# Performance work log

Hardware: AMD Instinct MI355X
Metric: run time of the kernel (lower is better)

Reference implementation:

```python
import jax, jax.numpy as jnp
import numpy as np

HEAD = 8

def setup_inputs() -> dict:
    key = jax.random.key(0)
    ks = jax.random.split(key, 11)
    B, C, W, H = 16, 512, 32, 32
    d, N = C // HEAD, W * H
    return {
        "x": jax.random.normal(ks[0], (B, C, W, H), jnp.float32),
        "Wq": jax.random.normal(ks[1], (C, C), jnp.float32) * 0.02,
        "bq": jax.random.normal(ks[2], (C,), jnp.float32) * 0.02,
        "Wk": jax.random.normal(ks[3], (C, C), jnp.float32) * 0.02,
        "bk": jax.random.normal(ks[4], (C,), jnp.float32) * 0.02,
        "Wv": jax.random.normal(ks[5], (C, C), jnp.float32) * 0.02,
        "bv": jax.random.normal(ks[6], (C,), jnp.float32) * 0.02,
        "rel_h": jax.random.normal(ks[7], (1, HEAD, d, 1, H), jnp.float32),
        "rel_w": jax.random.normal(ks[8], (1, HEAD, d, W, 1), jnp.float32),
        "reg_qk": jax.random.normal(ks[9], (1, N, N), jnp.float32),
        "reg_v": jax.random.normal(ks[10], (1, d, N), jnp.float32),
    }

def reference(x, Wq, bq, Wk, bk, Wv, bv, rel_h, rel_w, reg_qk, reg_v):
    B, C, W, H = x.shape
    head = HEAD
    d = C // head
    N = W * H
    def conv1x1(inp, Wt, b):  # 1x1 conv == per-pixel linear
        return jnp.einsum('bchw,oc->bohw', inp, Wt) + b[None, :, None, None]
    q = conv1x1(x, Wq, bq).reshape(B, head, d, N)
    k = conv1x1(x, Wk, bk).reshape(B, head, d, N)
    v = conv1x1(x, Wv, bv).reshape(B, head, d, N)
    # content-content: q^T k -> [B, head, N, N]
    cc = jnp.einsum('bhdn,bhdm->bhnm', q, k)
    # content-position: (rel_h + rel_w) broadcast to [1, head, d, W, H] -> [head, N, d]
    pos = (rel_h + rel_w).reshape(head, d, N)
    cp = jnp.einsum('hdn,bhdm->bhnm', pos, q)
    energy = cc + cp  # [B, head, N, N]
    n_reg = reg_qk.shape[0]
    energy = jnp.concatenate(
        [energy, jnp.broadcast_to(reg_qk[None], (B, n_reg, N, N))], axis=1)
    v_all = jnp.concatenate(
        [v, jnp.broadcast_to(reg_v[None], (B, n_reg, d, N))], axis=1)
    attn = jax.nn.softmax(energy, axis=-1)  # [B, head+n_reg, N, N]
    # v @ attn^T
    out = jnp.einsum('bgdn,bgmn->bgdm', v_all, attn)
    out = out[:, :head].reshape(B, C, W, H)
    return out + x
```

## Files before the change

kernel.cpp:

```cpp
#include <hip/hip_runtime.h>

#define BB   16
#define HEADS 8
#define DH   64
#define NSP  1024
#define CCH  512

typedef unsigned int   u32;
typedef unsigned short u16;
typedef __attribute__((ext_vector_type(8))) short  short8;
typedef __attribute__((ext_vector_type(4))) float  floatx4;

#if defined(__has_builtin)
#if __has_builtin(__builtin_amdgcn_exp2f)
#define EXP2F(x) __builtin_amdgcn_exp2f(x)
#else
#define EXP2F(x) exp2f(x)
#endif
#else
#define EXP2F(x) exp2f(x)
#endif

__device__ __forceinline__ u16 f2b(float f) {
  u32 x = __float_as_uint(f);
  x = x + 0x7fffu + ((x >> 16) & 1u);
  return (u16)(x >> 16);
}

__device__ __forceinline__ u32 pkbf(float lo, float hi) {
  return __builtin_amdgcn_perm(__float_as_uint(hi) + 0x8000u,
                               __float_as_uint(lo) + 0x8000u, 0x07060302u);
}

__device__ __forceinline__ void gload_lds16(const u16* g, u16* l) {
  __builtin_amdgcn_global_load_lds((const __attribute__((address_space(1))) u32*)g,
                                   (__attribute__((address_space(3))) u32*)l, 16, 0, 0);
}

__global__ __launch_bounds__(256) void prep_all(const float* __restrict__ x,
                                                const float* __restrict__ Wq,
                                                const float* __restrict__ Wk,
                                                const float* __restrict__ Wv,
                                                const float* __restrict__ rel_h,
                                                const float* __restrict__ rel_w,
                                                u16* __restrict__ wbf,
                                                u16* __restrict__ pos,
                                                u16* __restrict__ xt) {
  __shared__ float ld[64][68];
  int bid = blockIdx.x;
  int t = threadIdx.x;
  if (bid < 768) {
    int idx = bid * 256 + t;
    int which = idx >> 16;
    int r4 = (idx & 65535) * 4;
    const float* src = which == 0 ? Wq : which == 1 ? Wk : Wv;
    float4 v = *(const float4*)&src[r4];
    ushort4 s;
    s.x = f2b(v.x); s.y = f2b(v.y); s.z = f2b(v.z); s.w = f2b(v.w);
    *(ushort4*)&wbf[(which << 18) + r4] = s;
  } else if (bid < 2816) {
    int idx = (bid - 768) * 256 + t;
    int dd = idx & 63;
    int n  = (idx >> 6) & 1023;
    int h  = idx >> 16;
    int ww = n >> 5, hh = n & 31;
    float v = rel_h[(h * 64 + dd) * 32 + hh] + rel_w[(h * 64 + dd) * 32 + ww];
    pos[idx] = f2b(v);
  } else {
    int bid2 = bid - 2816;
    int ntile = bid2 & 15, ctile = (bid2 >> 4) & 7, b = bid2 >> 7;
    const float* xb = x + (((size_t)b * CCH + ctile * 64) << 10) + ntile * 64;
#pragma unroll
    for (int p = 0; p < 4; ++p) {
      int c = p * 16 + (t >> 4), n4 = (t & 15) * 4;
      float4 v = *(const float4*)&xb[((size_t)c << 10) + n4];
      ld[c][n4 + 0] = v.x; ld[c][n4 + 1] = v.y; ld[c][n4 + 2] = v.z; ld[c][n4 + 3] = v.w;
    }
    __syncthreads();
    u16* xo = xt + (((size_t)b << 10) + ntile * 64) * CCH + ctile * 64;
#pragma unroll
    for (int p = 0; p < 2; ++p) {
      int id = p * 256 + t;
      int n = id >> 3, c8 = (id & 7) * 8;
      ushort4 s0, s1;
      s0.x = f2b(ld[c8 + 0][n]); s0.y = f2b(ld[c8 + 1][n]);
      s0.z = f2b(ld[c8 + 2][n]); s0.w = f2b(ld[c8 + 3][n]);
      s1.x = f2b(ld[c8 + 4][n]); s1.y = f2b(ld[c8 + 5][n]);
      s1.z = f2b(ld[c8 + 6][n]); s1.w = f2b(ld[c8 + 7][n]);
      *(ushort4*)&xo[(size_t)n * CCH + c8] = s0;
      *(ushort4*)&xo[(size_t)n * CCH + c8 + 4] = s1;
    }
  }
}

__global__ __launch_bounds__(256, 2) void qkv_fused(const u16* __restrict__ wbf,
                                                    const u16* __restrict__ xt,
                                                    const float* __restrict__ bq,
                                                    const float* __restrict__ bk,
                                                    const float* __restrict__ bv,
                                                    u16* __restrict__ qw,
                                                    u16* __restrict__ kw,
                                                    u16* __restrict__ vtw) {
  int ntile = blockIdx.x, otile = blockIdx.y, b = blockIdx.z;
  int o0 = otile * 64, n0 = ntile * 128;

  __shared__ __align__(16) u16 smem[2 * 20480];

  int t = threadIdx.x;
  int w = t >> 6, lane = t & 63;
  int l15 = lane & 15, quad = lane >> 4;
  int srow = lane >> 3, sc = lane & 7;
  int scc = (sc ^ srow) << 3;

  floatx4 aq[8], ak[8], av[8];
#pragma unroll
  for (int i = 0; i < 8; ++i) {
    aq[i] = (floatx4){0.f, 0.f, 0.f, 0.f};
    ak[i] = (floatx4){0.f, 0.f, 0.f, 0.f};
    av[i] = (floatx4){0.f, 0.f, 0.f, 0.f};
  }

  auto stage = [&](int k0, int buf) {
    u16* base = smem + buf * 20480;
#pragma unroll
    for (int p = 0; p < 10; ++p) {
      int g0 = w * 80 + p * 8;
      if (g0 < 192) {
        int which = g0 >> 6;
        int r0 = g0 & 63;
        gload_lds16(wbf + ((size_t)which << 18) + (size_t)(o0 + r0 + srow) * CCH + k0 + scc,
                    base + which * 4096 + r0 * 64);
      } else {
        int r0 = g0 - 192;
        gload_lds16(xt + (size_t)(b * 1024 + n0 + r0 + srow) * CCH + k0 + scc,
                    base + 12288 + r0 * 64);
      }
    }
  };

  int rs = l15 & 7;
  int c0 = (quad ^ rs) << 3;
  int c1 = ((4 + quad) ^ rs) << 3;
  int wrow = (w * 16 + l15) * 64;

  stage(0, 0);

  for (int ki = 0; ki < 8; ++ki) {
    __syncthreads();
    if (ki < 7) stage((ki + 1) * 64, (ki + 1) & 1);

    u16* base = smem + (ki & 1) * 20480;
    u16* Xb = base + 12288;
#pragma unroll
    for (int ks = 0; ks < 2; ++ks) {
      int cc = ks ? c1 : c0;
      short8 fq = *(short8*)&base[wrow + cc];
      short8 fk = *(short8*)&base[4096 + wrow + cc];
      short8 fv = *(short8*)&base[8192 + wrow + cc];
#pragma unroll
      for (int ns = 0; ns < 8; ++ns) {
        short8 fx = *(short8*)&Xb[(ns * 16 + l15) * 64 + cc];
        aq[ns] = __builtin_amdgcn_mfma_f32_16x16x32_bf16(fq, fx, aq[ns], 0, 0, 0);
        ak[ns] = __builtin_amdgcn_mfma_f32_16x16x32_bf16(fk, fx, ak[ns], 0, 0, 0);
        av[ns] = __builtin_amdgcn_mfma_f32_16x16x32_bf16(fx, fv, av[ns], 0, 0, 0);
      }
    }
  }

  __syncthreads();
  u16* epQ = smem;
  u16* epK = smem + 9216;
  u16* epV = smem + 18432;
  {
    int ob = o0 + w * 16 + quad * 4;
    float q0 = bq[ob], q1 = bq[ob + 1], q2 = bq[ob + 2], q3 = bq[ob + 3];
    float k0b = bk[ob], k1b = bk[ob + 1], k2b = bk[ob + 2], k3b = bk[ob + 3];
    float vb = bv[o0 + w * 16 + l15];
#pragma unroll
    for (int ns = 0; ns < 8; ++ns) {
      int n = ns * 16 + l15;
      uint2 pk;
      pk.x = pkbf(aq[ns][0] + q0, aq[ns][1] + q1);
      pk.y = pkbf(aq[ns][2] + q2, aq[ns][3] + q3);
      *(uint2*)&epQ[n * 72 + w * 16 + quad * 4] = pk;
      pk.x = pkbf(ak[ns][0] + k0b, ak[ns][1] + k1b);
      pk.y = pkbf(ak[ns][2] + k2b, ak[ns][3] + k3b);
      *(uint2*)&epK[n * 72 + w * 16 + quad * 4] = pk;
      pk.x = pkbf(av[ns][0] + vb, av[ns][1] + vb);
      pk.y = pkbf(av[ns][2] + vb, av[ns][3] + vb);
      *(uint2*)&epV[(w * 16 + l15) * 136 + ns * 16 + quad * 4] = pk;
    }
  }
  __syncthreads();
  int h = otile;
  {
    int row = t >> 1, half = t & 1;
    size_t gb = ((size_t)(b * HEADS + h) * NSP + n0 + row) * 64 + half * 32;
#pragma unroll
    for (int i = 0; i < 4; ++i)
      *(uint4*)&qw[gb + i * 8] = *(uint4*)&epQ[row * 72 + half * 32 + i * 8];
#pragma unroll
    for (int i = 0; i < 4; ++i)
      *(uint4*)&kw[gb + i * 8] = *(uint4*)&epK[row * 72 + half * 32 + i * 8];
  }
  {
    int row = t >> 2, q4 = t & 3;
#pragma unroll
    for (int i = 0; i < 4; ++i) {
      int nl = q4 * 32 + i * 8;
      int n = n0 + nl;
      int ntl = n >> 6, nn = n & 63;
      *(uint4*)&vtw[(((size_t)(b * HEADS + h) * 16 + ntl) * 64 + row) * 64 + nn]
          = *(uint4*)&epV[row * 136 + nl];
    }
  }
}

__global__ __launch_bounds__(256, 2) void attn_mfma(const u16* __restrict__ qw,
                                                    const u16* __restrict__ kw,
                                                    const u16* __restrict__ vtw,
                                                    const u16* __restrict__ pos,
                                                    const float* __restrict__ x,
                                                    float* __restrict__ out) {
  int bh = blockIdx.x, mtile = blockIdx.y;
  int b = bh >> 3, h = bh & 7;
  __shared__ __align__(16) u16 smem_u16[34816];
  u16* pt = smem_u16 + 24576;

  int t = threadIdx.x;
  int w = t >> 6, lane = t & 63;
  int l15 = lane & 15, quad = lane >> 4;
  size_t bhs = (size_t)bh;

  short8 qa[4][2], pa[4][2];
  {
    const short* qg = (const short*)qw + (bhs * NSP + mtile * 256 + w * 64) * 64;
    const short* pg = (const short*)pos + ((size_t)h * NSP + mtile * 256 + w * 64) * 64;
#pragma unroll
    for (int msub = 0; msub < 4; ++msub)
#pragma unroll
      for (int ks = 0; ks < 2; ++ks) {
        int off = (msub * 16 + l15) * 64 + ks * 32 + quad * 8;
        qa[msub][ks] = *(const short8*)(qg + off);
        pa[msub][ks] = *(const short8*)(pg + off);
      }
  }

  floatx4 oacc[4][4];
  float lsum[4] = {0.f, 0.f, 0.f, 0.f};
#pragma unroll
  for (int i = 0; i < 4; ++i)
#pragma unroll
    for (int j = 0; j < 4; ++j) oacc[i][j] = (floatx4){0.f, 0.f, 0.f, 0.f};

  const u16* kg  = kw + bhs * NSP * 64;
  const u16* qgn = qw + bhs * NSP * 64;
  const u16* vg  = vtw + bhs * 16 * 4096;
  u16* ptw = pt + w * 2560;
  int srow = lane >> 3, sc = lane & 7;

  int rs = l15 & 7;
  int c0 = (quad ^ rs) << 3;
  int c1 = ((4 + quad) ^ rs) << 3;

  auto stage = [&](int nt, int buf) {
    u16* kt = smem_u16 + buf * 12288;
    u16* qt = kt + 4096;
    u16* vt = qt + 4096;
#pragma unroll
    for (int p = 0; p < 2; ++p) {
      int r0 = w * 16 + p * 8;
      int row = r0 + srow;
      int swz = ((sc ^ (row & 7)) << 3);
      gload_lds16(kg + (nt * 64 + row) * 64 + swz, &kt[r0 * 64]);
      gload_lds16(qgn + (nt * 64 + row) * 64 + swz, &qt[r0 * 64]);
      gload_lds16(vg + (size_t)nt * 4096 + row * 64 + swz, &vt[r0 * 64]);
    }
  };

  stage(0, 0);
  stage(1, 1);

  for (int nt = 0; nt < 16; ++nt) {
    if (nt < 15) asm volatile("s_waitcnt vmcnt(6)" ::: "memory");
    else         asm volatile("s_waitcnt vmcnt(0)" ::: "memory");
    __builtin_amdgcn_s_barrier();
    __builtin_amdgcn_sched_barrier(0);

    u16* kt = smem_u16 + (nt & 1) * 12288;
    u16* qt = kt + 4096;
    u16* vt = qt + 4096;

#pragma unroll
    for (int half = 0; half < 2; ++half) {
#pragma unroll
      for (int nblk2 = 0; nblk2 < 2; ++nblk2) {
        int nblk = half * 2 + nblk2;
        int rb = (nblk * 16 + l15) * 64;
        short8 kb0 = *(short8*)&kt[rb + c0];
        short8 kb1 = *(short8*)&kt[rb + c1];
        short8 qb0 = *(short8*)&qt[rb + c0];
        short8 qb1 = *(short8*)&qt[rb + c1];
        floatx4 sc4[4];
        __builtin_amdgcn_s_setprio(1);
#pragma unroll
        for (int msub = 0; msub < 4; ++msub) {
          floatx4 c = (floatx4){0.f, 0.f, 0.f, 0.f};
          c = __builtin_amdgcn_mfma_f32_16x16x32_bf16(kb0, qa[msub][0], c, 0, 0, 0);
          c = __builtin_amdgcn_mfma_f32_16x16x32_bf16(kb1, qa[msub][1], c, 0, 0, 0);
          c = __builtin_amdgcn_mfma_f32_16x16x32_bf16(qb0, pa[msub][0], c, 0, 0, 0);
          c = __builtin_amdgcn_mfma_f32_16x16x32_bf16(qb1, pa[msub][1], c, 0, 0, 0);
          sc4[msub] = c;
        }
        __builtin_amdgcn_s_setprio(0);
#pragma unroll
        for (int msub = 0; msub < 4; ++msub) {
          float p0 = EXP2F(fmaf(sc4[msub][0], 1.44269504f, -11.5415603f));
          float p1 = EXP2F(fmaf(sc4[msub][1], 1.44269504f, -11.5415603f));
          float p2 = EXP2F(fmaf(sc4[msub][2], 1.44269504f, -11.5415603f));
          float p3 = EXP2F(fmaf(sc4[msub][3], 1.44269504f, -11.5415603f));
          lsum[msub] += (p0 + p1) + (p2 + p3);
          uint2 pk;
          pk.x = pkbf(p0, p1);
          pk.y = pkbf(p2, p3);
          *(uint2*)&ptw[(msub * 16 + l15) * 40 + nblk2 * 16 + quad * 4] = pk;
        }
      }
      short8 pB[4];
#pragma unroll
      for (int msub = 0; msub < 4; ++msub)
        pB[msub] = *(short8*)&ptw[(msub * 16 + l15) * 40 + quad * 8];
      __builtin_amdgcn_s_setprio(1);
#pragma unroll
      for (int dd = 0; dd < 4; ++dd) {
        int row = dd * 16 + l15;
        short8 vb = *(short8*)&vt[row * 64 + (((half * 4 + quad) ^ (row & 7)) << 3)];
#pragma unroll
        for (int msub = 0; msub < 4; ++msub)
          oacc[msub][dd] = __builtin_amdgcn_mfma_f32_16x16x32_bf16(vb, pB[msub], oacc[msub][dd], 0, 0, 0);
      }
      __builtin_amdgcn_s_setprio(0);
    }

    if (nt < 14) {
      __builtin_amdgcn_sched_barrier(0);
      __builtin_amdgcn_s_barrier();
      stage(nt + 2, nt & 1);
    }
  }

  float rinv[4];
#pragma unroll
  for (int msub = 0; msub < 4; ++msub) {
    float l = lsum[msub];
    l += __shfl_xor(l, 16);
    l += __shfl_xor(l, 32);
    rinv[msub] = 1.0f / l;
  }

  __syncthreads();
  float* ot = (float*)smem_u16 + w * 2304;
  int l8 = lane & 7, lr = lane >> 3;
#pragma unroll
  for (int mh = 0; mh < 2; ++mh) {
#pragma unroll
    for (int ms2 = 0; ms2 < 2; ++ms2) {
      int msub = mh * 2 + ms2;
#pragma unroll
      for (int dd = 0; dd < 4; ++dd)
#pragma unroll
        for (int r = 0; r < 4; ++r)
          ot[(dd * 16 + quad * 4 + r) * 36 + ms2 * 16 + l15] = oacc[msub][dd][r] * rinv[msub];
    }
#pragma unroll
    for (int pass = 0; pass < 8; ++pass) {
      int dd = pass * 8 + lr;
      float4 o4 = *(float4*)&ot[dd * 36 + l8 * 4];
      size_t off = (((size_t)b * CCH + h * DH + dd) << 10) + mtile * 256 + w * 64 + mh * 32 + l8 * 4;
      float4 xv = *(const float4*)&x[off];
      o4.x += xv.x; o4.y += xv.y; o4.z += xv.z; o4.w += xv.w;
      *(float4*)&out[off] = o4;
    }
  }
}

extern "C" void kernel_launch(void* const* d_in, const int* in_sizes, int n_in,
                              void* d_out, int out_size, void* d_ws, size_t ws_size,
                              hipStream_t stream) {
  const float* x     = (const float*)d_in[0];
  const float* Wq    = (const float*)d_in[1];
  const float* bq    = (const float*)d_in[2];
  const float* Wk    = (const float*)d_in[3];
  const float* bk    = (const float*)d_in[4];
  const float* Wv    = (const float*)d_in[5];
  const float* bv    = (const float*)d_in[6];
  const float* rel_h = (const float*)d_in[7];
  const float* rel_w = (const float*)d_in[8];
  float* out = (float*)d_out;

  char* ws = (char*)d_ws;
  u16* qw   = (u16*)(ws);
  u16* kw   = (u16*)(ws + ((size_t)16 << 20));
  u16* vtw  = (u16*)(ws + ((size_t)32 << 20));
  u16* pos  = (u16*)(ws + ((size_t)48 << 20));
  u16* wbf  = (u16*)(ws + ((size_t)49 << 20));
  u16* xt   = (u16*)d_out;

  hipLaunchKernelGGL(prep_all, dim3(4864), dim3(256), 0, stream,
                     x, Wq, Wk, Wv, rel_h, rel_w, wbf, pos, xt);
  hipLaunchKernelGGL(qkv_fused, dim3(8, 8, 16), dim3(256), 0, stream,
                     wbf, xt, bq, bk, bv, qw, kw, vtw);
  hipLaunchKernelGGL(attn_mfma, dim3(128, 4), dim3(256), 0, stream,
                     qw, kw, vtw, pos, x, out);
}
```

Baseline: 209.2 us.

## Triple-buffer attention tiles, use permlane swaps for P, pipeline projection loads

The attention kernel moves from double to triple buffering of K/Q/V tiles. The next stage is issued right after a single barrier per iteration, which removes the second barrier. The P-matrix reshuffle into MFMA B-operand layout now uses permlane32/permlane16 swaps in registers instead of a round trip through LDS. The projection GEMM gains a two-deep prefetch with explicit vmcnt waits and raised MFMA priority. The extra LDS buffer may reduce occupancy, and the register permutation logic adds VALU work.

```diff
diff --git a/kernel.cpp b/kernel.cpp
--- a/kernel.cpp
+++ b/kernel.cpp
@@ -10,6 +10,7 @@
 typedef unsigned short u16;
 typedef __attribute__((ext_vector_type(8))) short  short8;
 typedef __attribute__((ext_vector_type(4))) float  floatx4;
+typedef __attribute__((ext_vector_type(2))) unsigned uint2v;
 
 #if defined(__has_builtin)
 #if __has_builtin(__builtin_amdgcn_exp2f)
@@ -17,6 +18,12 @@
 #else
 #define EXP2F(x) exp2f(x)
 #endif
+#if __has_builtin(__builtin_amdgcn_permlane32_swap)
+#define HAVE_PL32 1
+#endif
+#if __has_builtin(__builtin_amdgcn_permlane16_swap)
+#define HAVE_PL16 1
+#endif
 #else
 #define EXP2F(x) exp2f(x)
 #endif
@@ -35,6 +42,28 @@
 __device__ __forceinline__ void gload_lds16(const u16* g, u16* l) {
   __builtin_amdgcn_global_load_lds((const __attribute__((address_space(1))) u32*)g,
                                    (__attribute__((address_space(3))) u32*)l, 16, 0, 0);
+}
+
+__device__ __forceinline__ void lane32_swap(u32 a, u32 b, u32& ap, u32& bp, bool hi32) {
+#ifdef HAVE_PL32
+  uint2v r = __builtin_amdgcn_permlane32_swap(a, b, false, false);
+  ap = r.x; bp = r.y;
+  (void)hi32;
+#else
+  u32 sb = (u32)__shfl_xor((int)b, 32);
+  u32 sa = (u32)__shfl_xor((int)a, 32);
+  ap = hi32 ? sb : a;
+  bp = hi32 ? b : sa;
+#endif
+}
+
+__device__ __forceinline__ u32 lane16_xor(u32 x, bool qodd) {
+#ifdef HAVE_PL16
+  uint2v r = __builtin_amdgcn_permlane16_swap(x, x, false, false);
+  return qodd ? r.x : r.y;
+#else
+  return (u32)__shfl_xor((int)x, 16);
+#endif
 }
 
 __global__ __launch_bounds__(256) void prep_all(const float* __restrict__ x,
@@ -144,13 +173,17 @@
   int wrow = (w * 16 + l15) * 64;
 
   stage(0, 0);
+  stage(64, 1);
 
   for (int ki = 0; ki < 8; ++ki) {
-    __syncthreads();
-    if (ki < 7) stage((ki + 1) * 64, (ki + 1) & 1);
+    if (ki < 7) asm volatile("s_waitcnt vmcnt(10)" ::: "memory");
+    else        asm volatile("s_waitcnt vmcnt(0)" ::: "memory");
+    __builtin_amdgcn_s_barrier();
+    __builtin_amdgcn_sched_barrier(0);
 
     u16* base = smem + (ki & 1) * 20480;
     u16* Xb = base + 12288;
+    __builtin_amdgcn_s_setprio(1);
 #pragma unroll
     for (int ks = 0; ks < 2; ++ks) {
       int cc = ks ? c1 : c0;
@@ -164,6 +197,13 @@
         ak[ns] = __builtin_amdgcn_mfma_f32_16x16x32_bf16(fk, fx, ak[ns], 0, 0, 0);
         av[ns] = __builtin_amdgcn_mfma_f32_16x16x32_bf16(fx, fv, av[ns], 0, 0, 0);
       }
+    }
+    __builtin_amdgcn_s_setprio(0);
+
+    if (ki < 6) {
+      __builtin_amdgcn_sched_barrier(0);
+      __builtin_amdgcn_s_barrier();
+      stage((ki + 2) * 64, ki & 1);
     }
   }
 
@@ -224,12 +264,13 @@
                                                     float* __restrict__ out) {
   int bh = blockIdx.x, mtile = blockIdx.y;
   int b = bh >> 3, h = bh & 7;
-  __shared__ __align__(16) u16 smem_u16[34816];
-  u16* pt = smem_u16 + 24576;
+  __shared__ __align__(16) u16 smem_u16[36864];
 
   int t = threadIdx.x;
   int w = t >> 6, lane = t & 63;
   int l15 = lane & 15, quad = lane >> 4;
+  bool qodd = (quad & 1) != 0;
+  bool hi32 = lane >= 32;
   size_t bhs = (size_t)bh;
 
   short8 qa[4][2], pa[4][2];
@@ -256,7 +297,6 @@
   const u16* kg  = kw + bhs * NSP * 64;
   const u16* qgn = qw + bhs * NSP * 64;
   const u16* vg  = vtw + bhs * 16 * 4096;
-  u16* ptw = pt + w * 2560;
   int srow = lane >> 3, sc = lane & 7;
 
   int rs = l15 & 7;
@@ -282,17 +322,24 @@
   stage(1, 1);
 
   for (int nt = 0; nt < 16; ++nt) {
-    if (nt < 15) asm volatile("s_waitcnt vmcnt(6)" ::: "memory");
-    else         asm volatile("s_waitcnt vmcnt(0)" ::: "memory");
     __builtin_amdgcn_s_barrier();
+    if (nt < 14) {
+      stage(nt + 2, (nt + 2) % 3);
+      asm volatile("s_waitcnt vmcnt(12)" ::: "memory");
+    } else if (nt == 14) {
+      asm volatile("s_waitcnt vmcnt(6)" ::: "memory");
+    } else {
+      asm volatile("s_waitcnt vmcnt(0)" ::: "memory");
+    }
     __builtin_amdgcn_sched_barrier(0);
 
-    u16* kt = smem_u16 + (nt & 1) * 12288;
+    u16* kt = smem_u16 + (nt % 3) * 12288;
     u16* qt = kt + 4096;
     u16* vt = qt + 4096;
 
 #pragma unroll
     for (int half = 0; half < 2; ++half) {
+      u32 Wd[4][4];
 #pragma unroll
       for (int nblk2 = 0; nblk2 < 2; ++nblk2) {
         int nblk = half * 2 + nblk2;
@@ -320,16 +367,25 @@
           float p2 = EXP2F(fmaf(sc4[msub][2], 1.44269504f, -11.5415603f));
           float p3 = EXP2F(fmaf(sc4[msub][3], 1.44269504f, -11.5415603f));
           lsum[msub] += (p0 + p1) + (p2 + p3);
-          uint2 pk;
-          pk.x = pkbf(p0, p1);
-          pk.y = pkbf(p2, p3);
-          *(uint2*)&ptw[(msub * 16 + l15) * 40 + nblk2 * 16 + quad * 4] = pk;
+          Wd[msub][nblk2 * 2 + 0] = pkbf(p0, p1);
+          Wd[msub][nblk2 * 2 + 1] = pkbf(p2, p3);
         }
       }
       short8 pB[4];
 #pragma unroll
-      for (int msub = 0; msub < 4; ++msub)
-        pB[msub] = *(short8*)&ptw[(msub * 16 + l15) * 40 + quad * 8];
+      for (int msub = 0; msub < 4; ++msub) {
+        u32 A0p, B0p, A1p, B1p;
+        lane32_swap(Wd[msub][0], Wd[msub][2], A0p, B0p, hi32);
+        lane32_swap(Wd[msub][1], Wd[msub][3], A1p, B1p, hi32);
+        u32 G0 = lane16_xor(qodd ? A0p : B0p, qodd);
+        u32 G1 = lane16_xor(qodd ? A1p : B1p, qodd);
+        union { u32 u[4]; short8 s; } cvt;
+        cvt.u[0] = qodd ? G0 : A0p;
+        cvt.u[1] = qodd ? G1 : A1p;
+        cvt.u[2] = qodd ? B0p : G0;
+        cvt.u[3] = qodd ? B1p : G1;
+        pB[msub] = cvt.s;
+      }
       __builtin_amdgcn_s_setprio(1);
 #pragma unroll
       for (int dd = 0; dd < 4; ++dd) {
@@ -340,12 +396,6 @@
           oacc[msub][dd] = __builtin_amdgcn_mfma_f32_16x16x32_bf16(vb, pB[msub], oacc[msub][dd], 0, 0, 0);
       }
       __builtin_amdgcn_s_setprio(0);
-    }
-
-    if (nt < 14) {
-      __builtin_amdgcn_sched_barrier(0);
-      __builtin_amdgcn_s_barrier();
-      stage(nt + 2, nt & 1);
     }
   }
 
```

New measurement: 206.8 us. Within noise of the previous version (-1.2%).
